# Performance work log

Measured on AMD Instinct MI355X. Metric: run time of the kernel, lower is better.

The kernel has to match this reference:

```python
import jax, jax.numpy as jnp
import numpy as np
from jax import lax


def setup_inputs() -> dict:
    key = jax.random.key(0)
    k1, k2, k3 = jax.random.split(key, 3)
    B, K, H, W = 16, 11, 128, 128
    pred = jax.random.normal(k1, (B, K * 7, H, W), dtype=jnp.float32)
    gt = jax.random.normal(k2, (B, K, 7), dtype=jnp.float32)
    heatmap = jax.random.normal(k3, (B, K, H, W), dtype=jnp.float32)
    return {"pred": pred, "gt": gt, "heatmap": heatmap}


def reference(pred, gt, heatmap):
    B, K, H, W = heatmap.shape
    # AvgPool2d(kernel=3, stride=1, pad=1), count_include_pad=True (torch default) -> divide by 9 everywhere
    pooled = lax.reduce_window(
        heatmap, 0.0, lax.add,
        window_dimensions=(1, 1, 3, 3),
        window_strides=(1, 1, 1, 1),
        padding=((0, 0), (0, 0), (1, 1), (1, 1)),
    ) / 9.0
    # per (batch, gt-box) argmax over flattened HxW map
    index = jnp.argmax(pooled.reshape(B, K, H * W), axis=-1)  # [B, K]
    m = H  # faithful to original: x = index // m, y = index % m with m = size[2]
    x = index // m
    y = index % m
    # gather pred[b, k*7:(k+1)*7, x, y]
    predk = pred.reshape(B, K, 7, H, W)
    b_idx = jnp.arange(B)[:, None, None]          # [B,1,1]
    k_idx = jnp.arange(K)[None, :, None]          # [1,K,1]
    c_idx = jnp.arange(7)[None, None, :]          # [1,1,7]
    vals = predk[b_idx, k_idx, c_idx, x[..., None], y[..., None]]  # [B,K,7]
    diff = vals - gt[:, :, :7]
    class_loss = jnp.sum(diff * diff, axis=-1)    # MSE(reduction='sum') per (b,k)
    return class_loss.mean(axis=1)                # [B]
```

## Files before the change

### kernel.cpp

```cpp
#include <hip/hip_runtime.h>

#define HW    128
#define NPIX  16384
#define KBOX  11
#define NCH   7
#define NMAP  176
#define TILES 4
#define TROWS 32
#define LROW  136
#define LROWS 34
#define LSLOT (LROWS * (LROW / 4))
#define NLD   5

__global__ __launch_bounds__(256) void fused_label_loss(
    const float* __restrict__ pred,
    const float* __restrict__ gt,
    const float* __restrict__ heatmap,
    float* __restrict__ out)
{
    __shared__ float sm[2][LROWS * LROW];
    __shared__ float wv[4];
    __shared__ int   wi[4];
    __shared__ int   sIdx;

    const int bk  = blockIdx.x;
    const int b   = bk / KBOX;
    const int tid = threadIdx.x;
    const float* base = heatmap + (size_t)bk * NPIX;

    auto loadSlot = [&](int t, int idx) -> float4 {
        const int row = idx / (LROW / 4);
        const int sc  = (idx - row * (LROW / 4)) * 4;
        const int gr  = t * TROWS - 1 + row;
        float4 v = make_float4(0.f, 0.f, 0.f, 0.f);
        if (sc >= 4 && sc <= 128 && (unsigned)gr < (unsigned)HW)
            v = *(const float4*)(base + ((size_t)gr << 7) + (sc - 4));
        return v;
    };

    float4 regs[NLD];
    #pragma unroll
    for (int i = 0; i < NLD; ++i) {
        const int idx = tid + i * 256;
        regs[i] = (idx < LSLOT) ? loadSlot(0, idx) : make_float4(0.f, 0.f, 0.f, 0.f);
    }
    #pragma unroll
    for (int i = 0; i < NLD; ++i) {
        const int idx = tid + i * 256;
        if (idx < LSLOT) *(float4*)(sm[0] + idx * 4) = regs[i];
    }
    __syncthreads();

    float best = -INFINITY;
    int bestIdx = 0;

    for (int t = 0; t < TILES; ++t) {
        if (t + 1 < TILES) {
            #pragma unroll
            for (int i = 0; i < NLD; ++i) {
                const int idx = tid + i * 256;
                regs[i] = (idx < LSLOT) ? loadSlot(t + 1, idx)
                                        : make_float4(0.f, 0.f, 0.f, 0.f);
            }
        }

        const float* s = sm[t & 1];
        #pragma unroll
        for (int i = 0; i < 4; ++i) {
            const int q  = tid + i * 256;
            const int lr = q >> 5;
            const int c  = (q & 31) << 2;
            float4 ps = make_float4(0.f, 0.f, 0.f, 0.f);
            #pragma unroll
            for (int dr = 0; dr < 3; ++dr) {
                const float* rp = s + (lr + dr) * LROW + 4 + c;
                const float4 v = *(const float4*)rp;
                const float l = rp[-1];
                const float r = rp[4];
                ps.x += l   + v.x + v.y;
                ps.y += v.x + v.y + v.z;
                ps.z += v.y + v.z + v.w;
                ps.w += v.z + v.w + r;
            }
            ps.x *= (1.f / 9.f); ps.y *= (1.f / 9.f);
            ps.z *= (1.f / 9.f); ps.w *= (1.f / 9.f);
            const int pb = (t * TROWS + lr) * HW + c;
            if (ps.x > best) { best = ps.x; bestIdx = pb;     }
            if (ps.y > best) { best = ps.y; bestIdx = pb + 1; }
            if (ps.z > best) { best = ps.z; bestIdx = pb + 2; }
            if (ps.w > best) { best = ps.w; bestIdx = pb + 3; }
        }

        if (t + 1 < TILES) {
            #pragma unroll
            for (int i = 0; i < NLD; ++i) {
                const int idx = tid + i * 256;
                if (idx < LSLOT) *(float4*)(sm[(t + 1) & 1] + idx * 4) = regs[i];
            }
        }
        __syncthreads();
    }

    #pragma unroll
    for (int off = 32; off > 0; off >>= 1) {
        const float ov = __shfl_down(best, off, 64);
        const int   oi = __shfl_down(bestIdx, off, 64);
        if (ov > best || (ov == best && oi < bestIdx)) { best = ov; bestIdx = oi; }
    }
    if ((tid & 63) == 0) { wv[tid >> 6] = best; wi[tid >> 6] = bestIdx; }
    __syncthreads();

    if (tid == 0) {
        best = wv[0]; bestIdx = wi[0];
        #pragma unroll
        for (int w = 1; w < 4; ++w) {
            if (wv[w] > best || (wv[w] == best && wi[w] < bestIdx)) {
                best = wv[w]; bestIdx = wi[w];
            }
        }
        sIdx = bestIdx;
    }
    __syncthreads();

    float sq = 0.f;
    if (tid < NCH) {
        const float pv = pred[((size_t)(bk * NCH + tid)) * NPIX + sIdx];
        const float d  = pv - gt[(size_t)bk * NCH + tid];
        sq = d * d;
    }
    if (tid < 64) {
        sq += __shfl_down(sq, 4, 64);
        sq += __shfl_down(sq, 2, 64);
        sq += __shfl_down(sq, 1, 64);
        if (tid == 0) atomicAdd(out + b, sq * (1.0f / KBOX));
    }
}

extern "C" void kernel_launch(void* const* d_in, const int* in_sizes, int n_in,
                              void* d_out, int out_size, void* d_ws, size_t ws_size,
                              hipStream_t stream) {
    const float* pred    = (const float*)d_in[0];
    const float* gt      = (const float*)d_in[1];
    const float* heatmap = (const float*)d_in[2];
    float* out = (float*)d_out;

    fused_label_loss<<<dim3(NMAP), dim3(256), 0, stream>>>(pred, gt, heatmap, out);
}
```

Measured before the change: 115.0 us.

## Split pool-argmax into 1408 segment blocks plus finalize kernel, use shuffles for halos

Each heatmap map is now split into 8 row segments handled by separate blocks, giving 1408 blocks instead of 176 so more of the GPU's compute units are occupied. The 3x3 pooling now reads rows straight into registers and fetches neighbouring column values with wavefront shuffles instead of going through double-buffered shared memory. A second small kernel combines the per-segment partial argmax results and computes the loss. The cost is an extra kernel launch, a workspace round trip, and some duplicated halo-row loads.

Measured after the change: 115.5 us. No clear change (+0.4%).

```diff
diff --git a/kernel.cpp b/kernel.cpp
--- a/kernel.cpp
+++ b/kernel.cpp
@@ -5,135 +5,134 @@
 #define KBOX  11
 #define NCH   7
 #define NMAP  176
-#define TILES 4
-#define TROWS 32
-#define LROW  136
-#define LROWS 34
-#define LSLOT (LROWS * (LROW / 4))
-#define NLD   5
+#define SEGS  8
+#define SROWS 16
+#define GRID1 (NMAP * SEGS)
 
-__global__ __launch_bounds__(256) void fused_label_loss(
-    const float* __restrict__ pred,
-    const float* __restrict__ gt,
+__global__ __launch_bounds__(256) void pool_argmax_part(
     const float* __restrict__ heatmap,
-    float* __restrict__ out)
+    uint2* __restrict__ part)
 {
-    __shared__ float sm[2][LROWS * LROW];
-    __shared__ float wv[4];
-    __shared__ int   wi[4];
-    __shared__ int   sIdx;
+    const int blk = blockIdx.x;
+    const int map = blk >> 3;
+    const int seg = blk & 7;
+    const float* base = heatmap + (size_t)map * NPIX;
 
-    const int bk  = blockIdx.x;
-    const int b   = bk / KBOX;
-    const int tid = threadIdx.x;
-    const float* base = heatmap + (size_t)bk * NPIX;
+    const int t  = threadIdx.x;
+    const int lc = t & 31;
+    const int c  = lc << 2;
+    const int g  = t >> 5;
+    const int r0 = seg * SROWS + g * 2;
 
-    auto loadSlot = [&](int t, int idx) -> float4 {
-        const int row = idx / (LROW / 4);
-        const int sc  = (idx - row * (LROW / 4)) * 4;
-        const int gr  = t * TROWS - 1 + row;
-        float4 v = make_float4(0.f, 0.f, 0.f, 0.f);
-        if (sc >= 4 && sc <= 128 && (unsigned)gr < (unsigned)HW)
-            v = *(const float4*)(base + ((size_t)gr << 7) + (sc - 4));
-        return v;
-    };
+    float4 rv[4];
+    #pragma unroll
+    for (int i = 0; i < 4; ++i) {
+        const int rr = r0 - 1 + i;
+        rv[i] = ((unsigned)rr < (unsigned)HW)
+              ? *(const float4*)(base + ((size_t)rr << 7) + c)
+              : make_float4(0.f, 0.f, 0.f, 0.f);
+    }
 
-    float4 regs[NLD];
+    float lv[4], rvx[4];
     #pragma unroll
-    for (int i = 0; i < NLD; ++i) {
-        const int idx = tid + i * 256;
-        regs[i] = (idx < LSLOT) ? loadSlot(0, idx) : make_float4(0.f, 0.f, 0.f, 0.f);
+    for (int i = 0; i < 4; ++i) {
+        const float lu = __shfl_up(rv[i].w, 1, 32);
+        const float rd = __shfl_down(rv[i].x, 1, 32);
+        lv[i]  = (lc == 0)  ? 0.f : lu;
+        rvx[i] = (lc == 31) ? 0.f : rd;
     }
-    #pragma unroll
-    for (int i = 0; i < NLD; ++i) {
-        const int idx = tid + i * 256;
-        if (idx < LSLOT) *(float4*)(sm[0] + idx * 4) = regs[i];
-    }
-    __syncthreads();
+
+    const float4 mid = make_float4(rv[1].x + rv[2].x, rv[1].y + rv[2].y,
+                                   rv[1].z + rv[2].z, rv[1].w + rv[2].w);
+    const float4 cs0 = make_float4(mid.x + rv[0].x, mid.y + rv[0].y,
+                                   mid.z + rv[0].z, mid.w + rv[0].w);
+    const float4 cs1 = make_float4(mid.x + rv[3].x, mid.y + rv[3].y,
+                                   mid.z + rv[3].z, mid.w + rv[3].w);
+    const float ml = lv[1] + lv[2],  csl0 = ml + lv[0],  csl1 = ml + lv[3];
+    const float mr = rvx[1] + rvx[2], csr0 = mr + rvx[0], csr1 = mr + rvx[3];
 
     float best = -INFINITY;
-    int bestIdx = 0;
-
-    for (int t = 0; t < TILES; ++t) {
-        if (t + 1 < TILES) {
-            #pragma unroll
-            for (int i = 0; i < NLD; ++i) {
-                const int idx = tid + i * 256;
-                regs[i] = (idx < LSLOT) ? loadSlot(t + 1, idx)
-                                        : make_float4(0.f, 0.f, 0.f, 0.f);
-            }
-        }
-
-        const float* s = sm[t & 1];
-        #pragma unroll
-        for (int i = 0; i < 4; ++i) {
-            const int q  = tid + i * 256;
-            const int lr = q >> 5;
-            const int c  = (q & 31) << 2;
-            float4 ps = make_float4(0.f, 0.f, 0.f, 0.f);
-            #pragma unroll
-            for (int dr = 0; dr < 3; ++dr) {
-                const float* rp = s + (lr + dr) * LROW + 4 + c;
-                const float4 v = *(const float4*)rp;
-                const float l = rp[-1];
-                const float r = rp[4];
-                ps.x += l   + v.x + v.y;
-                ps.y += v.x + v.y + v.z;
-                ps.z += v.y + v.z + v.w;
-                ps.w += v.z + v.w + r;
-            }
-            ps.x *= (1.f / 9.f); ps.y *= (1.f / 9.f);
-            ps.z *= (1.f / 9.f); ps.w *= (1.f / 9.f);
-            const int pb = (t * TROWS + lr) * HW + c;
-            if (ps.x > best) { best = ps.x; bestIdx = pb;     }
-            if (ps.y > best) { best = ps.y; bestIdx = pb + 1; }
-            if (ps.z > best) { best = ps.z; bestIdx = pb + 2; }
-            if (ps.w > best) { best = ps.w; bestIdx = pb + 3; }
-        }
-
-        if (t + 1 < TILES) {
-            #pragma unroll
-            for (int i = 0; i < NLD; ++i) {
-                const int idx = tid + i * 256;
-                if (idx < LSLOT) *(float4*)(sm[(t + 1) & 1] + idx * 4) = regs[i];
-            }
-        }
-        __syncthreads();
+    int   bi   = 0;
+    const float inv9 = 1.0f / 9.0f;
+    {
+        const int pb = r0 * HW + c;
+        const float p0 = (csl0  + cs0.x + cs0.y) * inv9;
+        const float p1 = (cs0.x + cs0.y + cs0.z) * inv9;
+        const float p2 = (cs0.y + cs0.z + cs0.w) * inv9;
+        const float p3 = (cs0.z + cs0.w + csr0 ) * inv9;
+        if (p0 > best) { best = p0; bi = pb;     }
+        if (p1 > best) { best = p1; bi = pb + 1; }
+        if (p2 > best) { best = p2; bi = pb + 2; }
+        if (p3 > best) { best = p3; bi = pb + 3; }
+    }
+    {
+        const int pb = (r0 + 1) * HW + c;
+        const float p0 = (csl1  + cs1.x + cs1.y) * inv9;
+        const float p1 = (cs1.x + cs1.y + cs1.z) * inv9;
+        const float p2 = (cs1.y + cs1.z + cs1.w) * inv9;
+        const float p3 = (cs1.z + cs1.w + csr1 ) * inv9;
+        if (p0 > best) { best = p0; bi = pb;     }
+        if (p1 > best) { best = p1; bi = pb + 1; }
+        if (p2 > best) { best = p2; bi = pb + 2; }
+        if (p3 > best) { best = p3; bi = pb + 3; }
     }
 
     #pragma unroll
     for (int off = 32; off > 0; off >>= 1) {
         const float ov = __shfl_down(best, off, 64);
-        const int   oi = __shfl_down(bestIdx, off, 64);
-        if (ov > best || (ov == best && oi < bestIdx)) { best = ov; bestIdx = oi; }
+        const int   oi = __shfl_down(bi,   off, 64);
+        if (ov > best || (ov == best && oi < bi)) { best = ov; bi = oi; }
     }
-    if ((tid & 63) == 0) { wv[tid >> 6] = best; wi[tid >> 6] = bestIdx; }
+
+    __shared__ float wv[4];
+    __shared__ int   wi[4];
+    if ((t & 63) == 0) { wv[t >> 6] = best; wi[t >> 6] = bi; }
     __syncthreads();
-
-    if (tid == 0) {
-        best = wv[0]; bestIdx = wi[0];
+    if (t == 0) {
         #pragma unroll
         for (int w = 1; w < 4; ++w) {
-            if (wv[w] > best || (wv[w] == best && wi[w] < bestIdx)) {
-                best = wv[w]; bestIdx = wi[w];
+            if (wv[w] > best || (wv[w] == best && wi[w] < bi)) {
+                best = wv[w]; bi = wi[w];
             }
         }
-        sIdx = bestIdx;
+        part[blk] = make_uint2(__float_as_uint(best), (unsigned)bi);
     }
-    __syncthreads();
+}
+
+__global__ __launch_bounds__(64) void finalize_loss(
+    const float* __restrict__ pred,
+    const float* __restrict__ gt,
+    const uint2* __restrict__ part,
+    float* __restrict__ out)
+{
+    const int map = blockIdx.x;
+    const int t   = threadIdx.x;
+
+    float v  = -INFINITY;
+    int   bi = 0;
+    if (t < SEGS) {
+        const uint2 p = part[map * SEGS + t];
+        v  = __uint_as_float(p.x);
+        bi = (int)p.y;
+    }
+    #pragma unroll
+    for (int off = 4; off > 0; off >>= 1) {
+        const float ov = __shfl_down(v,  off, 64);
+        const int   oi = __shfl_down(bi, off, 64);
+        if (ov > v || (ov == v && oi < bi)) { v = ov; bi = oi; }
+    }
+    const int idx = __shfl(bi, 0, 64);
 
     float sq = 0.f;
-    if (tid < NCH) {
-        const float pv = pred[((size_t)(bk * NCH + tid)) * NPIX + sIdx];
-        const float d  = pv - gt[(size_t)bk * NCH + tid];
+    if (t < NCH) {
+        const float pv = pred[(size_t)(map * NCH + t) * NPIX + idx];
+        const float d  = pv - gt[(size_t)map * NCH + t];
         sq = d * d;
     }
-    if (tid < 64) {
-        sq += __shfl_down(sq, 4, 64);
-        sq += __shfl_down(sq, 2, 64);
-        sq += __shfl_down(sq, 1, 64);
-        if (tid == 0) atomicAdd(out + b, sq * (1.0f / KBOX));
-    }
+    sq += __shfl_down(sq, 4, 64);
+    sq += __shfl_down(sq, 2, 64);
+    sq += __shfl_down(sq, 1, 64);
+    if (t == 0) atomicAdd(out + map / KBOX, sq * (1.0f / KBOX));
 }
 
 extern "C" void kernel_launch(void* const* d_in, const int* in_sizes, int n_in,
@@ -143,6 +142,8 @@
     const float* gt      = (const float*)d_in[1];
     const float* heatmap = (const float*)d_in[2];
     float* out = (float*)d_out;
+    uint2* part = (uint2*)d_ws;
 
-    fused_label_loss<<<dim3(NMAP), dim3(256), 0, stream>>>(pred, gt, heatmap, out);
+    pool_argmax_part<<<dim3(GRID1), dim3(256), 0, stream>>>(heatmap, part);
+    finalize_loss<<<dim3(NMAP), dim3(64), 0, stream>>>(pred, gt, part, out);
 }
```
